# Kernel tuning notes

Hardware: AMD Instinct MI355X
Metric: run time of the kernel (lower is better)

The kernel has to match this reference:

```python
import math
import jax, jax.numpy as jnp
import numpy as np

D_MODEL = 768
NUM_HEADS = 12
D_K = D_MODEL // NUM_HEADS
THETA = 10000.0
MAX_SEQ_LEN = 4096
BATCH = 1
SEQ_LEN = 4096


def setup_inputs() -> dict:
    key = jax.random.key(0)
    k0, k1, k2, k3, k4 = jax.random.split(key, 5)
    scale = 0.02
    return {
        "in_features": jax.random.normal(k0, (BATCH, SEQ_LEN, D_MODEL), jnp.float32),
        "token_positions": jnp.arange(SEQ_LEN, dtype=jnp.int32),
        "q_proj": jax.random.normal(k1, (D_MODEL, D_MODEL), jnp.float32) * scale,
        "k_proj": jax.random.normal(k2, (D_MODEL, D_MODEL), jnp.float32) * scale,
        "v_proj": jax.random.normal(k3, (D_MODEL, D_MODEL), jnp.float32) * scale,
        "o_proj": jax.random.normal(k4, (D_MODEL, D_MODEL), jnp.float32) * scale,
    }


def _apply_rope(x, token_positions):
    # x: (B, H, S, d_k) ; token_positions: (S,) int
    inv_freq = 1.0 / (THETA ** (jnp.arange(0, D_K, 2, dtype=jnp.float32) / D_K))  # (d_k//2,)
    pos = jnp.clip(token_positions, 0, MAX_SEQ_LEN - 1).astype(jnp.float32)
    freq = pos[:, None] * inv_freq[None, :]                 # (S, d_k//2)
    cos, sin = jnp.cos(freq), jnp.sin(freq)
    xr = x.reshape(*x.shape[:-1], D_K // 2, 2)              # interleaved pairs
    x0, x1 = xr[..., 0], xr[..., 1]                         # (B, H, S, d_k//2)
    x0r = x0 * cos - x1 * sin
    x1r = x0 * sin + x1 * cos
    return jnp.stack((x0r, x1r), axis=-1).reshape(x.shape)


def reference(in_features, token_positions, q_proj, k_proj, v_proj, o_proj):
    B, S, D = in_features.shape
    H, dk = NUM_HEADS, D_K

    def proj_heads(W):
        y = jnp.matmul(in_features, W.T)                    # (B, S, D)
        return y.reshape(B, S, H, dk).transpose(0, 2, 1, 3)  # (B, H, S, dk)

    Q = _apply_rope(proj_heads(q_proj), token_positions)
    K = _apply_rope(proj_heads(k_proj), token_positions)
    V = proj_heads(v_proj)

    score = jnp.einsum("bhqd,bhkd->bhqk", Q, K) / math.sqrt(dk)
    causal = jnp.triu(jnp.ones((S, S), dtype=bool), k=1)    # True above diagonal
    score = jnp.where(causal[None, None], -jnp.inf, score)
    attn = jax.nn.softmax(score, axis=-1)
    out = jnp.einsum("bhqk,bhkd->bhqd", attn, V)            # (B, H, S, dk)
    out = out.transpose(0, 2, 1, 3).reshape(B, S, D)
    return jnp.matmul(out, o_proj.T)
```

## Files before the change

kernel.cpp:

```cpp
#include <hip/hip_runtime.h>
#include <hip/hip_bf16.h>

#define S_LEN 4096
#define DM    768
#define NH    12
#define DKH   64

typedef __attribute__((ext_vector_type(8))) short short8;
typedef __attribute__((ext_vector_type(4))) float f32x4;

__device__ __forceinline__ short f2bf(float f) {
    union { float f; unsigned u; } v; v.f = f;
    unsigned r = (v.u + 0x7FFFu + ((v.u >> 16) & 1u)) >> 16;
    return (short)r;
}

#define MFMA16(a, b, c) __builtin_amdgcn_mfma_f32_16x16x32_bf16((a), (b), (c), 0, 0, 0)

__device__ __forceinline__ void cvt4(const float* __restrict__ s,
                                     short* __restrict__ d, int i) {
    float4 v = *reinterpret_cast<const float4*>(s + i);
    short4 o;
    o.x = f2bf(v.x); o.y = f2bf(v.y); o.z = f2bf(v.z); o.w = f2bf(v.w);
    *reinterpret_cast<short4*>(d + i) = o;
}

__global__ __launch_bounds__(256) void prep_k(
    const float* __restrict__ X, const float* __restrict__ Wq,
    const float* __restrict__ Wk, const float* __restrict__ Wv,
    const float* __restrict__ Wo, const int* __restrict__ pos,
    short* __restrict__ Xbf, short* __restrict__ Wqb, short* __restrict__ Wkb,
    short* __restrict__ Wvb, short* __restrict__ Wob, float2* __restrict__ rt) {
    const int bx = blockIdx.x, tid = threadIdx.x;
    if (bx < 3072)      cvt4(X,  Xbf, bx * 1024 + tid * 4);
    else if (bx < 3648) cvt4(Wq, Wqb, (bx - 3072) * 1024 + tid * 4);
    else if (bx < 4224) cvt4(Wk, Wkb, (bx - 3648) * 1024 + tid * 4);
    else if (bx < 4800) cvt4(Wv, Wvb, (bx - 4224) * 1024 + tid * 4);
    else if (bx < 5376) cvt4(Wo, Wob, (bx - 4800) * 1024 + tid * 4);
    else {
        int idx = (bx - 5376) * 256 + tid;
        int s = idx >> 5, i = idx & 31;
        int p = pos[s]; p = p < 0 ? 0 : (p > 4095 ? 4095 : p);
        double inv = pow(10000.0, -(double)i / 32.0);
        float ang = (float)((double)p * inv);
        rt[idx] = make_float2(cosf(ang), sinf(ang));
    }
}

__device__ __forceinline__ void gemm_mainloop(const short* __restrict__ A,
                                              const short* __restrict__ B,
                                              short* Al, short* Bl,
                                              int m0, int n0, int t,
                                              f32x4 acc[4][4]) {
    const int wave = t >> 6, lane = t & 63;
    const int wm = (wave >> 1) * 64, wn = (wave & 1) * 64;
    const int l15 = lane & 15, lg = lane >> 4;
    const int grow = lane >> 3;
    const int gch = (lane & 7) ^ grow;
    const int dsto = wave * 512 + lane * 8;
    for (int k0 = 0; k0 < DM; k0 += 64) {
        __syncthreads();
#pragma unroll
        for (int i = 0; i < 4; ++i) {
            int row = i * 32 + wave * 8 + grow;
            __builtin_amdgcn_global_load_lds(
                (const __attribute__((address_space(1))) void*)&A[(m0 + row) * DM + k0 + gch * 8],
                (__attribute__((address_space(3))) void*)(Al + i * 2048 + dsto), 16, 0, 0);
            __builtin_amdgcn_global_load_lds(
                (const __attribute__((address_space(1))) void*)&B[(n0 + row) * DM + k0 + gch * 8],
                (__attribute__((address_space(3))) void*)(Bl + i * 2048 + dsto), 16, 0, 0);
        }
        __syncthreads();
#pragma unroll
        for (int kh = 0; kh < 2; ++kh) {
            const int c8 = (kh * 4 + lg) ^ (l15 & 7);
            short8 af[4], bf[4];
#pragma unroll
            for (int m = 0; m < 4; ++m)
                af[m] = *reinterpret_cast<const short8*>(Al + (wm + m * 16 + l15) * 64 + c8 * 8);
#pragma unroll
            for (int n = 0; n < 4; ++n)
                bf[n] = *reinterpret_cast<const short8*>(Bl + (wn + n * 16 + l15) * 64 + c8 * 8);
#pragma unroll
            for (int m = 0; m < 4; ++m)
#pragma unroll
                for (int n = 0; n < 4; ++n)
                    acc[m][n] = MFMA16(af[m], bf[n], acc[m][n]);
        }
    }
}

__global__ __launch_bounds__(256) void gemm_qkv_k(
    const short* __restrict__ Xbf, const short* __restrict__ Wq,
    const short* __restrict__ Wk, const short* __restrict__ Wv,
    const float2* __restrict__ rt,
    short* __restrict__ Q, short* __restrict__ K, short* __restrict__ Vt) {
    __shared__ __align__(16) short Al[128 * 64];
    __shared__ __align__(16) short Bl[128 * 64];
    const int mat = blockIdx.z;
    const short* B = mat == 0 ? Wq : (mat == 1 ? Wk : Wv);
    const int m0 = blockIdx.y * 128, n0 = blockIdx.x * 128;
    const int t = threadIdx.x;
    f32x4 acc[4][4] = {};
    gemm_mainloop(Xbf, B, Al, Bl, m0, n0, t, acc);
    const int wave = t >> 6, lane = t & 63;
    const int wm = (wave >> 1) * 64, wn = (wave & 1) * 64;
    const int l15 = lane & 15, lg = lane >> 4;
    if (mat < 2) {
        short* Out = mat == 0 ? Q : K;
        const float qs = 0.125f * 1.44269504088896f;
#pragma unroll
        for (int m = 0; m < 4; ++m) {
#pragma unroll
            for (int n = 0; n < 4; ++n) {
                int col = n0 + wn + n * 16 + l15;
                int h = col >> 6, d = col & 63;
#pragma unroll
                for (int j = 0; j < 4; ++j) {
                    int srow = m0 + wm + m * 16 + lg * 4 + j;
                    float v = acc[m][n][j];
                    float other = __shfl_xor(v, 1);
                    float2 cs = rt[srow * 32 + (d >> 1)];
                    v = (d & 1) ? (other * cs.y + v * cs.x)
                                : (v * cs.x - other * cs.y);
                    if (mat == 0) v *= qs;
                    Out[(h * S_LEN + srow) * DKH + d] = f2bf(v);
                }
            }
        }
    } else {
#pragma unroll
        for (int m = 0; m < 4; ++m)
#pragma unroll
            for (int n = 0; n < 4; ++n) {
                int col = n0 + wn + n * 16 + l15;
                int h = col >> 6, d = col & 63;
                int srow0 = m0 + wm + m * 16 + lg * 4;
                short4 b;
                b.x = f2bf(acc[m][n][0]); b.y = f2bf(acc[m][n][1]);
                b.z = f2bf(acc[m][n][2]); b.w = f2bf(acc[m][n][3]);
                *reinterpret_cast<short4*>(&Vt[(size_t)(h * DKH + d) * S_LEN + srow0]) = b;
            }
    }
}

__global__ __launch_bounds__(256) void gemm_out_k(const short* __restrict__ Ab,
                                                  const short* __restrict__ Wo,
                                                  float* __restrict__ out) {
    __shared__ __align__(16) short Al[128 * 64];
    __shared__ __align__(16) short Bl[128 * 64];
    const int m0 = blockIdx.y * 128, n0 = blockIdx.x * 128;
    const int t = threadIdx.x;
    f32x4 acc[4][4] = {};
    gemm_mainloop(Ab, Wo, Al, Bl, m0, n0, t, acc);
    const int wave = t >> 6, lane = t & 63;
    const int wm = (wave >> 1) * 64, wn = (wave & 1) * 64;
    const int l15 = lane & 15, lg = lane >> 4;
#pragma unroll
    for (int m = 0; m < 4; ++m)
#pragma unroll
        for (int n = 0; n < 4; ++n)
#pragma unroll
            for (int j = 0; j < 4; ++j) {
                int srow = m0 + wm + m * 16 + lg * 4 + j;
                int col = n0 + wn + n * 16 + l15;
                out[srow * DM + col] = acc[m][n][j];
            }
}

__device__ __forceinline__ void stage64(const short* __restrict__ gRow0,
                                        int rowStride, short* lbuf,
                                        int wave, int lane) {
#pragma unroll
    for (int i = 0; i < 2; ++i) {
        int c = wave + i * 4;
        int row = c * 8 + (lane >> 3);
        int gch = (lane & 7) ^ (lane >> 3);
        const short* src = gRow0 + (long)row * rowStride + gch * 8;
        short* dst = lbuf + c * 512 + lane * 8;
        __builtin_amdgcn_global_load_lds(
            (const __attribute__((address_space(1))) void*)src,
            (__attribute__((address_space(3))) void*)dst, 16, 0, 0);
    }
}

__global__ __launch_bounds__(256) void attn_k(const short* __restrict__ Q,
                                              const short* __restrict__ K,
                                              const short* __restrict__ Vt,
                                              short* __restrict__ Aout) {
    const int bx = blockIdx.x;
    const int h = bx % NH;
    const int qb = (S_LEN / 64 - 1) - (bx / NH);
    const int t = threadIdx.x;
    const int wave = t >> 6, lane = t & 63;
    const int l15 = lane & 15, lg = lane >> 4;
    const int q0w = qb * 64 + wave * 16;

    __shared__ __align__(16) short KVl[2][2][64 * 64];
    __shared__ __align__(16) short Pl[4][16][76];

    const short* Kh = K + (size_t)h * S_LEN * DKH;
    const short* Vh = Vt + (size_t)h * DKH * S_LEN;

    short8 qf[2];
#pragma unroll
    for (int ks = 0; ks < 2; ++ks)
        qf[ks] = *reinterpret_cast<const short8*>(
            &Q[(h * S_LEN + q0w + l15) * DKH + ks * 32 + lg * 8]);

    f32x4 o[4] = {};
    float mrun = -1e30f, lpart = 0.f;
    const int nt = qb + 1;

    stage64(Kh, DKH, KVl[0][0], wave, lane);
    stage64(Vh, S_LEN, KVl[0][1], wave, lane);
    __syncthreads();

    for (int tile = 0; tile < nt; ++tile) {
        const int cur = tile & 1;
        if (tile + 1 < nt) {
            stage64(Kh + (size_t)(tile + 1) * 64 * DKH, DKH, KVl[cur ^ 1][0], wave, lane);
            stage64(Vh + (tile + 1) * 64, S_LEN, KVl[cur ^ 1][1], wave, lane);
        }
        __builtin_amdgcn_sched_barrier(0);
        const char* Kb = (const char*)KVl[cur][0];
        const char* Vb = (const char*)KVl[cur][1];

        f32x4 s[4] = {};
        __builtin_amdgcn_s_setprio(1);
#pragma unroll
        for (int ks = 0; ks < 2; ++ks)
#pragma unroll
            for (int n = 0; n < 4; ++n) {
                int r = n * 16 + l15;
                int c8 = (ks * 4 + lg) ^ (r & 7);
                short8 kf = *reinterpret_cast<const short8*>(Kb + r * 128 + c8 * 16);
                s[n] = MFMA16(kf, qf[ks], s[n]);
            }
        __builtin_amdgcn_s_setprio(0);

        if (tile == qb) {
            const int q = q0w + l15;
#pragma unroll
            for (int n = 0; n < 4; ++n)
#pragma unroll
                for (int j = 0; j < 4; ++j)
                    if (tile * 64 + n * 16 + lg * 4 + j > q) s[n][j] = -1e30f;
        }

        float mt = fmaxf(fmaxf(fmaxf(s[0][0], s[0][1]), fmaxf(s[0][2], s[0][3])),
                         fmaxf(fmaxf(s[1][0], s[1][1]), fmaxf(s[1][2], s[1][3])));
        mt = fmaxf(mt, fmaxf(fmaxf(fmaxf(s[2][0], s[2][1]), fmaxf(s[2][2], s[2][3])),
                             fmaxf(fmaxf(s[3][0], s[3][1]), fmaxf(s[3][2], s[3][3]))));

        if (__all(mt <= mrun + 8.f)) {
#pragma unroll
            for (int n = 0; n < 4; ++n)
#pragma unroll
                for (int j = 0; j < 4; ++j) {
                    float p = exp2f(s[n][j] - mrun);
                    s[n][j] = p;
                    lpart += p;
                }
        } else {
            float mm = fmaxf(mt, __shfl_xor(mt, 16));
            mm = fmaxf(mm, __shfl_xor(mm, 32));
            float mnew = fmaxf(mrun, mm);
            float alpha = exp2f(mrun - mnew);
            lpart *= alpha;
#pragma unroll
            for (int n = 0; n < 4; ++n)
#pragma unroll
                for (int j = 0; j < 4; ++j) {
                    float p = exp2f(s[n][j] - mnew);
                    s[n][j] = p;
                    lpart += p;
                }
#pragma unroll
            for (int n = 0; n < 4; ++n)
#pragma unroll
                for (int j = 0; j < 4; ++j) o[n][j] *= alpha;
            mrun = mnew;
        }

#pragma unroll
        for (int n = 0; n < 4; ++n) {
            unsigned p0, p1;
            asm("v_cvt_pk_bf16_f32 %0, %1, %2" : "=v"(p0) : "v"(s[n][0]), "v"(s[n][1]));
            asm("v_cvt_pk_bf16_f32 %0, %1, %2" : "=v"(p1) : "v"(s[n][2]), "v"(s[n][3]));
            uint2 w; w.x = p0; w.y = p1;
            *reinterpret_cast<uint2*>(&Pl[wave][l15][n * 16 + lg * 4]) = w;
        }

        __builtin_amdgcn_s_setprio(1);
#pragma unroll
        for (int ks = 0; ks < 2; ++ks) {
            short8 pa = *reinterpret_cast<const short8*>(
                &Pl[wave][l15][ks * 32 + lg * 8]);
#pragma unroll
            for (int n = 0; n < 4; ++n) {
                int r = n * 16 + l15;
                int c8 = (ks * 4 + lg) ^ (r & 7);
                short8 vf = *reinterpret_cast<const short8*>(Vb + r * 128 + c8 * 16);
                o[n] = MFMA16(vf, pa, o[n]);
            }
        }
        __builtin_amdgcn_s_setprio(0);

        asm volatile("s_waitcnt vmcnt(0)" ::: "memory");
        __builtin_amdgcn_sched_barrier(0);
        __builtin_amdgcn_s_barrier();
    }

    float lsum = lpart + __shfl_xor(lpart, 16);
    lsum += __shfl_xor(lsum, 32);
    float inv = 1.f / lsum;

    __syncthreads();
    float* Ol = (float*)&KVl[0][0][0] + wave * (16 * 68);
#pragma unroll
    for (int n = 0; n < 4; ++n) {
        float4 w;
        w.x = o[n][0] * inv; w.y = o[n][1] * inv;
        w.z = o[n][2] * inv; w.w = o[n][3] * inv;
        *reinterpret_cast<float4*>(&Ol[l15 * 68 + n * 16 + lg * 4]) = w;
    }
#pragma unroll
    for (int kk = 0; kk < 4; ++kk) {
        int r = lane >> 2, c0 = (lane & 3) * 4 + kk * 16;
        float4 v = *reinterpret_cast<const float4*>(&Ol[r * 68 + c0]);
        short4 b;
        b.x = f2bf(v.x); b.y = f2bf(v.y); b.z = f2bf(v.z); b.w = f2bf(v.w);
        *reinterpret_cast<short4*>(
            &Aout[(size_t)(q0w + r) * DM + h * DKH + c0]) = b;
    }
}

extern "C" void kernel_launch(void* const* d_in, const int* in_sizes, int n_in,
                              void* d_out, int out_size, void* d_ws, size_t ws_size,
                              hipStream_t stream) {
    const float* X  = (const float*)d_in[0];
    const int*   pos = (const int*)d_in[1];
    const float* Wq = (const float*)d_in[2];
    const float* Wk = (const float*)d_in[3];
    const float* Wv = (const float*)d_in[4];
    const float* Wo = (const float*)d_in[5];
    float* out = (float*)d_out;

    char* ws = (char*)d_ws;
    short* Xbf = (short*)ws;  ws += (size_t)S_LEN * DM * 2;
    short* Wqb = (short*)ws;  ws += (size_t)DM * DM * 2;
    short* Wkb = (short*)ws;  ws += (size_t)DM * DM * 2;
    short* Wvb = (short*)ws;  ws += (size_t)DM * DM * 2;
    short* Wob = (short*)ws;  ws += (size_t)DM * DM * 2;
    float2* rt = (float2*)ws; ws += (size_t)S_LEN * 32 * 8;
    short* Qb  = (short*)ws;  ws += (size_t)NH * S_LEN * DKH * 2;
    short* Kb  = (short*)ws;  ws += (size_t)NH * S_LEN * DKH * 2;
    short* Vtb = (short*)ws;  ws += (size_t)NH * S_LEN * DKH * 2;
    short* Ab  = (short*)ws;  ws += (size_t)S_LEN * DM * 2;

    prep_k<<<5888, 256, 0, stream>>>(X, Wq, Wk, Wv, Wo, pos,
                                     Xbf, Wqb, Wkb, Wvb, Wob, rt);
    gemm_qkv_k<<<dim3(6, 32, 3), 256, 0, stream>>>(Xbf, Wqb, Wkb, Wvb, rt, Qb, Kb, Vtb);
    attn_k<<<dim3(64 * NH), 256, 0, stream>>>(Qb, Kb, Vtb, Ab);
    gemm_out_k<<<dim3(6, 32), 256, 0, stream>>>(Ab, Wob, out);
}
```

Baseline: 147.3 us.

## Double-buffer LDS tiles in GEMM mainloop to overlap global loads with MFMA

```diff
diff --git a/kernel.cpp b/kernel.cpp
--- a/kernel.cpp
+++ b/kernel.cpp
@@ -58,36 +58,57 @@
     const int grow = lane >> 3;
     const int gch = (lane & 7) ^ grow;
     const int dsto = wave * 512 + lane * 8;
-    for (int k0 = 0; k0 < DM; k0 += 64) {
-        __syncthreads();
-#pragma unroll
-        for (int i = 0; i < 4; ++i) {
-            int row = i * 32 + wave * 8 + grow;
-            __builtin_amdgcn_global_load_lds(
-                (const __attribute__((address_space(1))) void*)&A[(m0 + row) * DM + k0 + gch * 8],
-                (__attribute__((address_space(3))) void*)(Al + i * 2048 + dsto), 16, 0, 0);
-            __builtin_amdgcn_global_load_lds(
-                (const __attribute__((address_space(1))) void*)&B[(n0 + row) * DM + k0 + gch * 8],
-                (__attribute__((address_space(3))) void*)(Bl + i * 2048 + dsto), 16, 0, 0);
-        }
-        __syncthreads();
+
+#define GEMM_STAGE(k0, buf)                                                          \
+    {                                                                                \
+        _Pragma("unroll")                                                            \
+        for (int i = 0; i < 4; ++i) {                                                \
+            int row = i * 32 + wave * 8 + grow;                                      \
+            __builtin_amdgcn_global_load_lds(                                        \
+                (const __attribute__((address_space(1))) void*)                      \
+                    &A[(m0 + row) * DM + (k0) + gch * 8],                            \
+                (__attribute__((address_space(3))) void*)                            \
+                    (Al + (buf) * 8192 + i * 2048 + dsto), 16, 0, 0);                \
+            __builtin_amdgcn_global_load_lds(                                        \
+                (const __attribute__((address_space(1))) void*)                      \
+                    &B[(n0 + row) * DM + (k0) + gch * 8],                            \
+                (__attribute__((address_space(3))) void*)                            \
+                    (Bl + (buf) * 8192 + i * 2048 + dsto), 16, 0, 0);                \
+        }                                                                            \
+    }
+
+    GEMM_STAGE(0, 0);
+    asm volatile("s_waitcnt vmcnt(0)" ::: "memory");
+    __builtin_amdgcn_s_barrier();
+
+    const int NSTEP = DM / 64;
+    for (int step = 0; step < NSTEP; ++step) {
+        const int cur = step & 1;
+        if (step + 1 < NSTEP) GEMM_STAGE((step + 1) * 64, cur ^ 1);
+        __builtin_amdgcn_sched_barrier(0);
+        const short* Ab_ = Al + cur * 8192;
+        const short* Bb_ = Bl + cur * 8192;
 #pragma unroll
         for (int kh = 0; kh < 2; ++kh) {
             const int c8 = (kh * 4 + lg) ^ (l15 & 7);
             short8 af[4], bf[4];
 #pragma unroll
             for (int m = 0; m < 4; ++m)
-                af[m] = *reinterpret_cast<const short8*>(Al + (wm + m * 16 + l15) * 64 + c8 * 8);
-#pragma unroll
-            for (int n = 0; n < 4; ++n)
-                bf[n] = *reinterpret_cast<const short8*>(Bl + (wn + n * 16 + l15) * 64 + c8 * 8);
+                af[m] = *reinterpret_cast<const short8*>(Ab_ + (wm + m * 16 + l15) * 64 + c8 * 8);
+#pragma unroll
+            for (int n = 0; n < 4; ++n)
+                bf[n] = *reinterpret_cast<const short8*>(Bb_ + (wn + n * 16 + l15) * 64 + c8 * 8);
 #pragma unroll
             for (int m = 0; m < 4; ++m)
 #pragma unroll
                 for (int n = 0; n < 4; ++n)
                     acc[m][n] = MFMA16(af[m], bf[n], acc[m][n]);
         }
-    }
+        asm volatile("s_waitcnt vmcnt(0)" ::: "memory");
+        __builtin_amdgcn_sched_barrier(0);
+        __builtin_amdgcn_s_barrier();
+    }
+#undef GEMM_STAGE
 }
 
 __global__ __launch_bounds__(256) void gemm_qkv_k(
@@ -95,8 +116,8 @@
     const short* __restrict__ Wk, const short* __restrict__ Wv,
     const float2* __restrict__ rt,
     short* __restrict__ Q, short* __restrict__ K, short* __restrict__ Vt) {
-    __shared__ __align__(16) short Al[128 * 64];
-    __shared__ __align__(16) short Bl[128 * 64];
+    __shared__ __align__(16) short Al[2 * 128 * 64];
+    __shared__ __align__(16) short Bl[2 * 128 * 64];
     const int mat = blockIdx.z;
     const short* B = mat == 0 ? Wq : (mat == 1 ? Wk : Wv);
     const int m0 = blockIdx.y * 128, n0 = blockIdx.x * 128;
@@ -147,8 +168,8 @@
 __global__ __launch_bounds__(256) void gemm_out_k(const short* __restrict__ Ab,
                                                   const short* __restrict__ Wo,
                                                   float* __restrict__ out) {
-    __shared__ __align__(16) short Al[128 * 64];
-    __shared__ __align__(16) short Bl[128 * 64];
+    __shared__ __align__(16) short Al[2 * 128 * 64];
+    __shared__ __align__(16) short Bl[2 * 128 * 64];
     const int m0 = blockIdx.y * 128, n0 = blockIdx.x * 128;
     const int t = threadIdx.x;
     f32x4 acc[4][4] = {};
```

After: 147.7 us. About the same (+0.3%).
